# Kernel tuning notes

Hardware: AMD Instinct MI355X
Metric: run time of the kernel (lower is better)

## Reference

```python
import jax, jax.numpy as jnp
import numpy as np

H = 16   # heads
DK = 64  # d_model // heads
LN_EPS = 1e-5


def setup_inputs() -> dict:
    key = jax.random.key(0)
    ks = jax.random.split(key, 6)
    bs, S, D = 2, 1024, 1024
    lim = 1.0 / np.sqrt(DK)  # torch Linear default init scale
    return {
        "context": jax.random.normal(ks[0], (bs, S, D), jnp.float32),
        "eos_mask": jnp.ones((bs, 1, S, S), jnp.bool_),
        "prior": jax.random.uniform(ks[1], (bs, H, S, S), jnp.float32),
        "ln_w": jnp.ones((D,), jnp.float32),
        "ln_b": jnp.zeros((D,), jnp.float32),
        "wk": jax.random.uniform(ks[2], (DK, DK), jnp.float32, -lim, lim),
        "bk": jax.random.uniform(ks[3], (DK,), jnp.float32, -lim, lim),
        "wq": jax.random.uniform(ks[4], (DK, DK), jnp.float32, -lim, lim),
        "bq": jax.random.uniform(ks[5], (DK,), jnp.float32, -lim, lim),
    }


def reference(context, eos_mask, prior, ln_w, ln_b, wk, bk, wq, bq):
    bs, S, D = context.shape
    # LayerNorm (torch uses biased variance)
    mu = context.mean(-1, keepdims=True)
    var = context.var(-1, keepdims=True)
    x = (context - mu) / jnp.sqrt(var + LN_EPS) * ln_w + ln_b
    # [bs, h, S, dk]
    x = x.reshape(bs, S, H, DK).transpose(0, 2, 1, 3)

    a = jnp.eye(S, k=1, dtype=jnp.float32)    # superdiagonal
    c = jnp.eye(S, k=-1, dtype=jnp.float32)   # subdiagonal
    eye = jnp.eye(S, dtype=jnp.float32)
    mask = eos_mask & ((a + c) > 0)           # [bs,1,S,S] tridiagonal (no diag)

    k = x @ wk.T + bk
    q = x @ wq.T + bq
    scores = jnp.einsum('bhqd,bhkd->bhqk', q, k) / DK
    scores = jnp.where(mask, scores, -10000.0)
    neibor = jax.nn.softmax(scores, axis=-1)
    # symmetrized geometric-mean neighbor attention
    neibor = jnp.sqrt(neibor * jnp.swapaxes(neibor, -2, -1) + 1e-4)
    neibor = prior + (1.0 - prior) * neibor

    tri = jnp.triu(jnp.ones((S, S), jnp.float32))  # incl. diag
    # keep log only on the superdiagonal, then prefix-sum via triu matmuls
    logn = jnp.where(a > 0, jnp.log(neibor + 1e-9), 0.0)
    t = logn @ tri                      # [bs,h,S,S]
    g = jnp.exp(jnp.matmul(tri, t))     # broadcasted [S,S] @ [bs,h,S,S]
    g = jnp.where((tri - eye) > 0, g, 0.0)  # keep strict upper triangle
    g = g + jnp.swapaxes(g, -2, -1) + jnp.where(eye > 0, neibor, 1e-4)
    return g, neibor


if __name__ == "__main__":
    out = reference(**setup_inputs())
    print(out[0].shape, out[1].shape)
```

## Files before the change

### kernel.cpp

```cpp
#include <hip/hip_runtime.h>
#include <hip/hip_bf16.h>

#define S 1024
#define H 16
#define BS 2
#define D 1024

typedef float f32x4 __attribute__((ext_vector_type(4)));

__global__ __launch_bounds__(256) void k_ln_prep(const float* __restrict__ ctx,
                                                 const float* __restrict__ wk,
                                                 const float* __restrict__ bk,
                                                 const float* __restrict__ wq,
                                                 const float* __restrict__ bq,
                                                 float* __restrict__ mean,
                                                 float* __restrict__ rstd,
                                                 float* __restrict__ Mt,
                                                 float* __restrict__ uvec) {
    __shared__ float sh[2 * 64 * 65];
    int t = threadIdx.x;
    int bid = blockIdx.x;

    if (bid >= BS * S) {
        int p = bid - BS * S;
        float* WqL = sh;
        float* WkL = sh + 64 * 65;
        for (int idx = t; idx < 4096; idx += 256) {
            int d = idx >> 6, c = idx & 63;
            WqL[d * 65 + c] = wq[idx];
            WkL[d * 65 + c] = wk[idx];
        }
        __syncthreads();
        int a = t & 63, sub = t >> 6;
        for (int ee = sub; ee < 16; ee += 4) {
            int e = p * 16 + ee;
            float acc = 0.0f;
            #pragma unroll 8
            for (int d = 0; d < 64; ++d) acc += WqL[d * 65 + a] * WkL[d * 65 + e];
            Mt[e * 64 + a] = acc;
        }
        if (p == 0 && t < 64) {
            float acc = 0.0f;
            #pragma unroll 8
            for (int d = 0; d < 64; ++d) acc += bq[d] * WkL[d * 65 + t];
            uvec[t] = acc;
        }
        return;
    }

    const float* x = ctx + (size_t)bid * D;
    float4 v = *(const float4*)(x + t * 4);
    float s = v.x + v.y + v.z + v.w;
    float sq = v.x * v.x + v.y * v.y + v.z * v.z + v.w * v.w;
    #pragma unroll
    for (int off = 32; off > 0; off >>= 1) {
        s += __shfl_down(s, off);
        sq += __shfl_down(sq, off);
    }
    float* ss = sh;
    float* sqs = sh + 4;
    int w = t >> 6;
    if ((t & 63) == 0) { ss[w] = s; sqs[w] = sq; }
    __syncthreads();
    if (t == 0) {
        float sum = ss[0] + ss[1] + ss[2] + ss[3];
        float sumsq = sqs[0] + sqs[1] + sqs[2] + sqs[3];
        float m = sum * (1.0f / D);
        float var = sumsq * (1.0f / D) - m * m;
        mean[bid] = m;
        rstd[bid] = rsqrtf(var + 1e-5f);
    }
}

#define XST 68
__global__ __launch_bounds__(256) void k_scores(const float* __restrict__ ctx,
                                                const float* __restrict__ mean,
                                                const float* __restrict__ rstd,
                                                const float* __restrict__ lnw,
                                                const float* __restrict__ lnb,
                                                const float* __restrict__ Mt,
                                                const float* __restrict__ uvec,
                                                float* __restrict__ p_up,
                                                float* __restrict__ p_dn) {
    int chunk = blockIdx.x;
    int bh = blockIdx.y;
    int b = bh >> 4, h = bh & 15;
    int r0 = chunk * 64;
    int t = threadIdx.x;
    int lane = t & 63, w = t >> 6;

    __shared__ float xs[72][XST];
    __shared__ float ts[72][XST];

    float Mreg[64];
    #pragma unroll
    for (int e = 0; e < 64; ++e) Mreg[e] = Mt[e * 64 + lane];

    for (int idx = t; idx < 72 * 64; idx += 256) {
        int lr = idx >> 6, c = idx & 63;
        int row = r0 - 1 + lr;
        float v = 0.0f;
        if (lr < 66 && row >= 0 && row < S) {
            float cv = ctx[((size_t)b * S + row) * D + h * 64 + c];
            v = (cv - mean[b * S + row]) * rstd[b * S + row] * lnw[h * 64 + c] + lnb[h * 64 + c];
        }
        xs[lr][c] = v;
    }
    __syncthreads();

    for (int s8 = w; s8 < 9; s8 += 4) {
        int rb = s8 * 8;
        float acc[8] = {0, 0, 0, 0, 0, 0, 0, 0};
        #pragma unroll
        for (int eq = 0; eq < 16; ++eq) {
            #pragma unroll
            for (int rr = 0; rr < 8; ++rr) {
                float4 xv = *(const float4*)&xs[rb + rr][eq * 4];
                acc[rr] += Mreg[eq * 4 + 0] * xv.x + Mreg[eq * 4 + 1] * xv.y +
                           Mreg[eq * 4 + 2] * xv.z + Mreg[eq * 4 + 3] * xv.w;
            }
        }
        #pragma unroll
        for (int rr = 0; rr < 8; ++rr) ts[rb + rr][lane] = acc[rr];
    }
    __syncthreads();

    {
        int l = w * 16 + (lane >> 2);
        int part = lane & 3;
        float diff = 0.0f;
        #pragma unroll
        for (int dq = 0; dq < 4; ++dq) {
            int d0 = part * 16 + dq * 4;
            float4 xi = *(const float4*)&xs[l + 1][d0];
            float4 t2 = *(const float4*)&ts[l + 2][d0];
            float4 t0 = *(const float4*)&ts[l][d0];
            float4 x2 = *(const float4*)&xs[l + 2][d0];
            float4 x0 = *(const float4*)&xs[l][d0];
            float4 uv = *(const float4*)&uvec[d0];
            diff += xi.x * (t2.x - t0.x) + uv.x * (x2.x - x0.x);
            diff += xi.y * (t2.y - t0.y) + uv.y * (x2.y - x0.y);
            diff += xi.z * (t2.z - t0.z) + uv.z * (x2.z - x0.z);
            diff += xi.w * (t2.w - t0.w) + uv.w * (x2.w - x0.w);
        }
        diff += __shfl_down(diff, 2);
        diff += __shfl_down(diff, 1);
        if (part == 0) {
            int i = r0 + l;
            float z = diff * (1.0f / 64.0f);
            float pu, pd;
            if (i == 0)          { pu = 1.0f; pd = 0.0f; }
            else if (i == S - 1) { pu = 0.0f; pd = 1.0f; }
            else {
                float ez = __expf(-z);
                pu = 1.0f / (1.0f + ez);
                pd = 1.0f - pu;
            }
            p_up[bh * S + i] = pu;
            p_dn[bh * S + i] = pd;
        }
    }
}

__global__ __launch_bounds__(1024) void k_scan(const float* __restrict__ p_up,
                                               const float* __restrict__ p_dn,
                                               const float* __restrict__ prior,
                                               float* __restrict__ n_up,
                                               float* __restrict__ C) {
    int bh = blockIdx.x;
    int t = threadIdx.x;
    float L = 0.0f;
    if (t > 0) {
        int i = t - 1;
        float nr = sqrtf(p_up[bh * S + i] * p_dn[bh * S + i + 1] + 1e-4f);
        n_up[bh * S + i] = nr;
        float pr = prior[((size_t)bh * S + i) * S + i + 1];
        float N = pr + (1.0f - pr) * nr;
        L = logf(N + 1e-9f);
    }
    int lane = t & 63, wid = t >> 6;
    float val = L;
    #pragma unroll
    for (int off = 1; off < 64; off <<= 1) {
        float v = __shfl_up(val, off, 64);
        if (lane >= off) val += v;
    }
    __shared__ float wsum[16];
    if (lane == 63) wsum[wid] = val;
    __syncthreads();
    if (t < 16) {
        float v2 = wsum[t];
        #pragma unroll
        for (int off = 1; off < 16; off <<= 1) {
            float x = __shfl_up(v2, off, 64);
            if (t >= off) v2 += x;
        }
        wsum[t] = v2;
    }
    __syncthreads();
    float base = (wid > 0) ? wsum[wid - 1] : 0.0f;
    C[bh * S + t] = base + val;
}

__global__ __launch_bounds__(256) void k_out(const float* __restrict__ prior,
                                             const float* __restrict__ n_up,
                                             const float* __restrict__ C,
                                             float* __restrict__ g_out,
                                             float* __restrict__ nb_out) {
    int bid = blockIdx.x;
    int bh = bid >> 10, i = bid & 1023;
    int t = threadIdx.x;
    size_t rowbase = (size_t)bid * S;
    float Ci = C[bh * S + i];
    float nup_i  = (i < S - 1) ? n_up[bh * S + i] : 0.0f;
    float nup_im = (i > 0)     ? n_up[bh * S + i - 1] : 0.0f;
    int j0 = t * 4;
    f32x4 p4 = __builtin_nontemporal_load((const f32x4*)(prior + rowbase + j0));
    float4 c4 = *(const float4*)(C + bh * S + j0);
    float pv[4] = {p4.x, p4.y, p4.z, p4.w};
    float cv[4] = {c4.x, c4.y, c4.z, c4.w};
    float gv[4], nv[4];
    #pragma unroll
    for (int l = 0; l < 4; ++l) {
        int j = j0 + l;
        float p = pv[l];
        float v = 0.01f;
        if (j == i + 1) v = nup_i;
        if (j == i - 1) v = nup_im;
        float nb = p + (1.0f - p) * v;
        nv[l] = nb;
        float gg;
        if (j == i) {
            gg = nb;
        } else {
            float dd = (j > i) ? (cv[l] - Ci) : (Ci - cv[l]);
            gg = __expf(dd) + 1e-4f;
        }
        gv[l] = gg;
    }
    f32x4 gq = {gv[0], gv[1], gv[2], gv[3]};
    f32x4 nq = {nv[0], nv[1], nv[2], nv[3]};
    __builtin_nontemporal_store(gq, (f32x4*)(g_out + rowbase + j0));
    __builtin_nontemporal_store(nq, (f32x4*)(nb_out + rowbase + j0));
}

extern "C" void kernel_launch(void* const* d_in, const int* in_sizes, int n_in,
                              void* d_out, int out_size, void* d_ws, size_t ws_size,
                              hipStream_t stream) {
    const float* ctx   = (const float*)d_in[0];
    const float* prior = (const float*)d_in[2];
    const float* lnw   = (const float*)d_in[3];
    const float* lnb   = (const float*)d_in[4];
    const float* wk    = (const float*)d_in[5];
    const float* bk    = (const float*)d_in[6];
    const float* wq    = (const float*)d_in[7];
    const float* bq    = (const float*)d_in[8];

    float* ws = (float*)d_ws;
    float* mean = ws;
    float* rstd = ws + 2048;
    float* Mt   = ws + 4096;
    float* uvec = ws + 8192;
    float* p_up = ws + 8448;
    float* p_dn = ws + 8448 + 32768;
    float* n_up = ws + 8448 + 65536;
    float* C    = ws + 8448 + 98304;

    float* g_out  = (float*)d_out;
    float* nb_out = (float*)d_out + (size_t)BS * H * S * S;

    k_ln_prep<<<BS * S + 4, 256, 0, stream>>>(ctx, wk, bk, wq, bq, mean, rstd, Mt, uvec);
    k_scores<<<dim3(16, BS * H), 256, 0, stream>>>(ctx, mean, rstd, lnw, lnb, Mt, uvec,
                                                   p_up, p_dn);
    k_scan<<<BS * H, 1024, 0, stream>>>(p_up, p_dn, prior, n_up, C);
    k_out<<<BS * H * S, 256, 0, stream>>>(prior, n_up, C, g_out, nb_out);
}
```

Before: 106.0 us.

## Fuse LayerNorm, weight product and scores into one kernel; batch output rows

```diff
diff --git a/kernel.cpp b/kernel.cpp
--- a/kernel.cpp
+++ b/kernel.cpp
@@ -5,160 +5,142 @@
 #define H 16
 #define BS 2
 #define D 1024
+#define CH 8
 
 typedef float f32x4 __attribute__((ext_vector_type(4)));
 
-__global__ __launch_bounds__(256) void k_ln_prep(const float* __restrict__ ctx,
-                                                 const float* __restrict__ wk,
-                                                 const float* __restrict__ bk,
-                                                 const float* __restrict__ wq,
-                                                 const float* __restrict__ bq,
-                                                 float* __restrict__ mean,
-                                                 float* __restrict__ rstd,
-                                                 float* __restrict__ Mt,
-                                                 float* __restrict__ uvec) {
-    __shared__ float sh[2 * 64 * 65];
-    int t = threadIdx.x;
-    int bid = blockIdx.x;
-
-    if (bid >= BS * S) {
-        int p = bid - BS * S;
-        float* WqL = sh;
-        float* WkL = sh + 64 * 65;
-        for (int idx = t; idx < 4096; idx += 256) {
-            int d = idx >> 6, c = idx & 63;
-            WqL[d * 65 + c] = wq[idx];
-            WkL[d * 65 + c] = wk[idx];
-        }
-        __syncthreads();
-        int a = t & 63, sub = t >> 6;
-        for (int ee = sub; ee < 16; ee += 4) {
-            int e = p * 16 + ee;
-            float acc = 0.0f;
-            #pragma unroll 8
-            for (int d = 0; d < 64; ++d) acc += WqL[d * 65 + a] * WkL[d * 65 + e];
-            Mt[e * 64 + a] = acc;
-        }
-        if (p == 0 && t < 64) {
-            float acc = 0.0f;
-            #pragma unroll 8
-            for (int d = 0; d < 64; ++d) acc += bq[d] * WkL[d * 65 + t];
-            uvec[t] = acc;
-        }
-        return;
-    }
-
-    const float* x = ctx + (size_t)bid * D;
-    float4 v = *(const float4*)(x + t * 4);
-    float s = v.x + v.y + v.z + v.w;
-    float sq = v.x * v.x + v.y * v.y + v.z * v.z + v.w * v.w;
-    #pragma unroll
-    for (int off = 32; off > 0; off >>= 1) {
-        s += __shfl_down(s, off);
-        sq += __shfl_down(sq, off);
-    }
-    float* ss = sh;
-    float* sqs = sh + 4;
-    int w = t >> 6;
-    if ((t & 63) == 0) { ss[w] = s; sqs[w] = sq; }
-    __syncthreads();
-    if (t == 0) {
-        float sum = ss[0] + ss[1] + ss[2] + ss[3];
-        float sumsq = sqs[0] + sqs[1] + sqs[2] + sqs[3];
-        float m = sum * (1.0f / D);
-        float var = sumsq * (1.0f / D) - m * m;
-        mean[bid] = m;
-        rstd[bid] = rsqrtf(var + 1e-5f);
-    }
-}
-
-#define XST 68
-__global__ __launch_bounds__(256) void k_scores(const float* __restrict__ ctx,
-                                                const float* __restrict__ mean,
-                                                const float* __restrict__ rstd,
-                                                const float* __restrict__ lnw,
-                                                const float* __restrict__ lnb,
-                                                const float* __restrict__ Mt,
-                                                const float* __restrict__ uvec,
-                                                float* __restrict__ p_up,
-                                                float* __restrict__ p_dn) {
-    int chunk = blockIdx.x;
-    int bh = blockIdx.y;
-    int b = bh >> 4, h = bh & 15;
-    int r0 = chunk * 64;
+__global__ __launch_bounds__(256) void k12(const float* __restrict__ ctx,
+                                           const float* __restrict__ lnw,
+                                           const float* __restrict__ lnb,
+                                           const float* __restrict__ wk,
+                                           const float* __restrict__ wq,
+                                           const float* __restrict__ bq,
+                                           float* __restrict__ p_up,
+                                           float* __restrict__ p_dn) {
+    __shared__ float Ml[64 * 65];
+    __shared__ float uw[64];
+    __shared__ float xs[CH + 2][1032];
+    __shared__ float ts[CH + 2][68];
+    __shared__ float mu[CH + 2], rs[CH + 2];
+    __shared__ float lw[1024], lb[1024];
+
     int t = threadIdx.x;
     int lane = t & 63, w = t >> 6;
-
-    __shared__ float xs[72][XST];
-    __shared__ float ts[72][XST];
-
+    int chunk = blockIdx.x, b = blockIdx.y;
+    int r0 = chunk * CH;
+
+    float* WqL = &xs[0][0];
+    float* WkL = &xs[0][0] + 4160;
+    for (int idx = t; idx < 4096; idx += 256) {
+        int d = idx >> 6, c = idx & 63;
+        WqL[d * 65 + c] = wq[idx];
+        WkL[d * 65 + c] = wk[idx];
+    }
+    ((f32x4*)lw)[t] = ((const f32x4*)lnw)[t];
+    ((f32x4*)lb)[t] = ((const f32x4*)lnb)[t];
+    __syncthreads();
+    for (int ee = 0; ee < 16; ++ee) {
+        int e = w * 16 + ee;
+        float acc = 0.0f;
+        #pragma unroll 8
+        for (int d = 0; d < 64; ++d) acc += WqL[d * 65 + lane] * WkL[d * 65 + e];
+        Ml[e * 65 + lane] = acc;
+    }
+    if (w == 0) {
+        float acc = 0.0f;
+        #pragma unroll 8
+        for (int d = 0; d < 64; ++d) acc += bq[d] * WkL[d * 65 + lane];
+        uw[lane] = acc;
+    }
+    __syncthreads();
+
+    #pragma unroll
+    for (int q = 0; q < CH + 2; ++q) {
+        int gr = r0 - 1 + q;
+        f32x4 v = {0.f, 0.f, 0.f, 0.f};
+        if (gr >= 0 && gr < S) v = ((const f32x4*)(ctx + ((size_t)b * S + gr) * D))[t];
+        *(f32x4*)&xs[q][t * 4] = v;
+    }
     float Mreg[64];
     #pragma unroll
-    for (int e = 0; e < 64; ++e) Mreg[e] = Mt[e * 64 + lane];
-
-    for (int idx = t; idx < 72 * 64; idx += 256) {
-        int lr = idx >> 6, c = idx & 63;
-        int row = r0 - 1 + lr;
-        float v = 0.0f;
-        if (lr < 66 && row >= 0 && row < S) {
-            float cv = ctx[((size_t)b * S + row) * D + h * 64 + c];
-            v = (cv - mean[b * S + row]) * rstd[b * S + row] * lnw[h * 64 + c] + lnb[h * 64 + c];
-        }
-        xs[lr][c] = v;
-    }
-    __syncthreads();
-
-    for (int s8 = w; s8 < 9; s8 += 4) {
-        int rb = s8 * 8;
-        float acc[8] = {0, 0, 0, 0, 0, 0, 0, 0};
-        #pragma unroll
-        for (int eq = 0; eq < 16; ++eq) {
+    for (int e = 0; e < 64; ++e) Mreg[e] = Ml[e * 65 + lane];
+    __syncthreads();
+
+    for (int q = w; q < CH + 2; q += 4) {
+        float s = 0.f, sq = 0.f;
+        #pragma unroll
+        for (int k = 0; k < 4; ++k) {
+            f32x4 v = *(const f32x4*)&xs[q][(lane + 64 * k) * 4];
+            s += v.x + v.y + v.z + v.w;
+            sq += v.x * v.x + v.y * v.y + v.z * v.z + v.w * v.w;
+        }
+        #pragma unroll
+        for (int off = 32; off > 0; off >>= 1) {
+            s += __shfl_down(s, off);
+            sq += __shfl_down(sq, off);
+        }
+        if (lane == 0) {
+            float m = s * (1.0f / D);
+            float var = sq * (1.0f / D) - m * m;
+            mu[q] = m;
+            rs[q] = rsqrtf(var + 1e-5f);
+        }
+    }
+    __syncthreads();
+
+    #pragma unroll
+    for (int q = 0; q < CH + 2; ++q) {
+        float m = mu[q], r = rs[q];
+        f32x4 v = *(const f32x4*)&xs[q][t * 4];
+        f32x4 wv = *(const f32x4*)&lw[t * 4];
+        f32x4 bv = *(const f32x4*)&lb[t * 4];
+        v.x = (v.x - m) * r * wv.x + bv.x;
+        v.y = (v.y - m) * r * wv.y + bv.y;
+        v.z = (v.z - m) * r * wv.z + bv.z;
+        v.w = (v.w - m) * r * wv.w + bv.w;
+        *(f32x4*)&xs[q][t * 4] = v;
+    }
+    __syncthreads();
+
+    for (int h = 0; h < H; ++h) {
+        int hc = h * 64;
+        for (int q = w; q < CH + 2; q += 4) {
+            float a0 = 0.f, a1 = 0.f, a2 = 0.f, a3 = 0.f;
             #pragma unroll
-            for (int rr = 0; rr < 8; ++rr) {
-                float4 xv = *(const float4*)&xs[rb + rr][eq * 4];
-                acc[rr] += Mreg[eq * 4 + 0] * xv.x + Mreg[eq * 4 + 1] * xv.y +
-                           Mreg[eq * 4 + 2] * xv.z + Mreg[eq * 4 + 3] * xv.w;
+            for (int eq = 0; eq < 16; ++eq) {
+                f32x4 xv = *(const f32x4*)&xs[q][hc + eq * 4];
+                a0 += Mreg[eq * 4 + 0] * xv.x;
+                a1 += Mreg[eq * 4 + 1] * xv.y;
+                a2 += Mreg[eq * 4 + 2] * xv.z;
+                a3 += Mreg[eq * 4 + 3] * xv.w;
             }
-        }
-        #pragma unroll
-        for (int rr = 0; rr < 8; ++rr) ts[rb + rr][lane] = acc[rr];
-    }
-    __syncthreads();
-
-    {
-        int l = w * 16 + (lane >> 2);
-        int part = lane & 3;
-        float diff = 0.0f;
-        #pragma unroll
-        for (int dq = 0; dq < 4; ++dq) {
-            int d0 = part * 16 + dq * 4;
-            float4 xi = *(const float4*)&xs[l + 1][d0];
-            float4 t2 = *(const float4*)&ts[l + 2][d0];
-            float4 t0 = *(const float4*)&ts[l][d0];
-            float4 x2 = *(const float4*)&xs[l + 2][d0];
-            float4 x0 = *(const float4*)&xs[l][d0];
-            float4 uv = *(const float4*)&uvec[d0];
-            diff += xi.x * (t2.x - t0.x) + uv.x * (x2.x - x0.x);
-            diff += xi.y * (t2.y - t0.y) + uv.y * (x2.y - x0.y);
-            diff += xi.z * (t2.z - t0.z) + uv.z * (x2.z - x0.z);
-            diff += xi.w * (t2.w - t0.w) + uv.w * (x2.w - x0.w);
-        }
-        diff += __shfl_down(diff, 2);
-        diff += __shfl_down(diff, 1);
-        if (part == 0) {
-            int i = r0 + l;
-            float z = diff * (1.0f / 64.0f);
-            float pu, pd;
-            if (i == 0)          { pu = 1.0f; pd = 0.0f; }
-            else if (i == S - 1) { pu = 0.0f; pd = 1.0f; }
-            else {
-                float ez = __expf(-z);
-                pu = 1.0f / (1.0f + ez);
-                pd = 1.0f - pu;
+            ts[q][lane] = (a0 + a1) + (a2 + a3);
+        }
+        __syncthreads();
+        for (int lr = 1 + w; lr <= CH; lr += 4) {
+            int i = r0 + lr - 1;
+            float xi = xs[lr][hc + lane];
+            float tp = ts[lr + 1][lane] - ts[lr - 1][lane];
+            float xd = xs[lr + 1][hc + lane] - xs[lr - 1][hc + lane];
+            float v = xi * tp + uw[lane] * xd;
+            #pragma unroll
+            for (int off = 32; off > 0; off >>= 1) v += __shfl_down(v, off);
+            if (lane == 0) {
+                float z = v * (1.0f / 64.0f);
+                float pu, pd;
+                if (i == 0)          { pu = 1.0f; pd = 0.0f; }
+                else if (i == S - 1) { pu = 0.0f; pd = 1.0f; }
+                else {
+                    float ez = __expf(-z);
+                    pu = 1.0f / (1.0f + ez);
+                    pd = 1.0f - pu;
+                }
+                int bh = b * H + h;
+                p_up[bh * S + i] = pu;
+                p_dn[bh * S + i] = pd;
             }
-            p_up[bh * S + i] = pu;
-            p_dn[bh * S + i] = pd;
-        }
+        }
+        __syncthreads();
     }
 }
 
@@ -207,41 +189,41 @@
                                              const float* __restrict__ C,
                                              float* __restrict__ g_out,
                                              float* __restrict__ nb_out) {
+    int t = threadIdx.x;
     int bid = blockIdx.x;
-    int bh = bid >> 10, i = bid & 1023;
-    int t = threadIdx.x;
-    size_t rowbase = (size_t)bid * S;
-    float Ci = C[bh * S + i];
-    float nup_i  = (i < S - 1) ? n_up[bh * S + i] : 0.0f;
-    float nup_im = (i > 0)     ? n_up[bh * S + i - 1] : 0.0f;
+    int bh = bid >> 7;
+    int i0 = (bid & 127) * 8;
     int j0 = t * 4;
-    f32x4 p4 = __builtin_nontemporal_load((const f32x4*)(prior + rowbase + j0));
-    float4 c4 = *(const float4*)(C + bh * S + j0);
-    float pv[4] = {p4.x, p4.y, p4.z, p4.w};
-    float cv[4] = {c4.x, c4.y, c4.z, c4.w};
-    float gv[4], nv[4];
-    #pragma unroll
-    for (int l = 0; l < 4; ++l) {
-        int j = j0 + l;
-        float p = pv[l];
-        float v = 0.01f;
-        if (j == i + 1) v = nup_i;
-        if (j == i - 1) v = nup_im;
-        float nb = p + (1.0f - p) * v;
-        nv[l] = nb;
-        float gg;
-        if (j == i) {
-            gg = nb;
-        } else {
-            float dd = (j > i) ? (cv[l] - Ci) : (Ci - cv[l]);
-            gg = __expf(dd) + 1e-4f;
-        }
-        gv[l] = gg;
-    }
-    f32x4 gq = {gv[0], gv[1], gv[2], gv[3]};
-    f32x4 nq = {nv[0], nv[1], nv[2], nv[3]};
-    __builtin_nontemporal_store(gq, (f32x4*)(g_out + rowbase + j0));
-    __builtin_nontemporal_store(nq, (f32x4*)(nb_out + rowbase + j0));
+    const float* Crow = C + bh * S;
+    f32x4 c4 = *(const f32x4*)(Crow + j0);
+    f32x4 ciA = *(const f32x4*)(Crow + i0);
+    f32x4 ciB = *(const f32x4*)(Crow + i0 + 4);
+    #pragma unroll
+    for (int r = 0; r < 8; ++r) {
+        int i = i0 + r;
+        float Ci = (r < 4) ? ciA[r] : ciB[r - 4];
+        size_t rowbase = ((size_t)bh * S + i) * S;
+        f32x4 p4 = __builtin_nontemporal_load((const f32x4*)(prior + rowbase + j0));
+        f32x4 nb, gg;
+        #pragma unroll
+        for (int l = 0; l < 4; ++l) {
+            nb[l] = fmaf(0.99f, p4[l], 0.01f);
+            gg[l] = __expf(-fabsf(c4[l] - Ci)) + 1e-4f;
+        }
+        if (i - 1 <= j0 + 3 && i + 1 >= j0) {
+            float nup_i  = (i < S - 1) ? n_up[bh * S + i] : 0.0f;
+            float nup_im = (i > 0)     ? n_up[bh * S + i - 1] : 0.0f;
+            #pragma unroll
+            for (int l = 0; l < 4; ++l) {
+                int j = j0 + l;
+                if (j == i + 1) nb[l] = p4[l] + (1.0f - p4[l]) * nup_i;
+                if (j == i - 1) nb[l] = p4[l] + (1.0f - p4[l]) * nup_im;
+                if (j == i)     gg[l] = nb[l];
+            }
+        }
+        __builtin_nontemporal_store(gg, (f32x4*)(g_out + rowbase + j0));
+        __builtin_nontemporal_store(nb, (f32x4*)(nb_out + rowbase + j0));
+    }
 }
 
 extern "C" void kernel_launch(void* const* d_in, const int* in_sizes, int n_in,
@@ -252,26 +234,19 @@
     const float* lnw   = (const float*)d_in[3];
     const float* lnb   = (const float*)d_in[4];
     const float* wk    = (const float*)d_in[5];
-    const float* bk    = (const float*)d_in[6];
     const float* wq    = (const float*)d_in[7];
     const float* bq    = (const float*)d_in[8];
 
     float* ws = (float*)d_ws;
-    float* mean = ws;
-    float* rstd = ws + 2048;
-    float* Mt   = ws + 4096;
-    float* uvec = ws + 8192;
-    float* p_up = ws + 8448;
-    float* p_dn = ws + 8448 + 32768;
-    float* n_up = ws + 8448 + 65536;
-    float* C    = ws + 8448 + 98304;
+    float* p_up = ws;
+    float* p_dn = ws + 32768;
+    float* n_up = ws + 65536;
+    float* C    = ws + 98304;
 
     float* g_out  = (float*)d_out;
     float* nb_out = (float*)d_out + (size_t)BS * H * S * S;
 
-    k_ln_prep<<<BS * S + 4, 256, 0, stream>>>(ctx, wk, bk, wq, bq, mean, rstd, Mt, uvec);
-    k_scores<<<dim3(16, BS * H), 256, 0, stream>>>(ctx, mean, rstd, lnw, lnb, Mt, uvec,
-                                                   p_up, p_dn);
+    k12<<<dim3(S / CH, BS), 256, 0, stream>>>(ctx, lnw, lnb, wk, wq, bq, p_up, p_dn);
     k_scan<<<BS * H, 1024, 0, stream>>>(p_up, p_dn, prior, n_up, C);
-    k_out<<<BS * H * S, 256, 0, stream>>>(prior, n_up, C, g_out, nb_out);
-}
+    k_out<<<BS * H * S / 8, 256, 0, stream>>>(prior, n_up, C, g_out, nb_out);
+}
```

New measurement: 133.4 us. +25.8%, slower.

## Fuse neighbor log computation into scores kernel and batch 8 rows per output block

Applied to the files above, without the earlier changes.

```diff
diff --git a/kernel.cpp b/kernel.cpp
--- a/kernel.cpp
+++ b/kernel.cpp
@@ -10,7 +10,6 @@
 
 __global__ __launch_bounds__(256) void k_ln_prep(const float* __restrict__ ctx,
                                                  const float* __restrict__ wk,
-                                                 const float* __restrict__ bk,
                                                  const float* __restrict__ wq,
                                                  const float* __restrict__ bq,
                                                  float* __restrict__ mean,
@@ -80,8 +79,9 @@
                                                 const float* __restrict__ lnb,
                                                 const float* __restrict__ Mt,
                                                 const float* __restrict__ uvec,
-                                                float* __restrict__ p_up,
-                                                float* __restrict__ p_dn) {
+                                                const float* __restrict__ prior,
+                                                float* __restrict__ n_up,
+                                                float* __restrict__ Lg) {
     int chunk = blockIdx.x;
     int bh = blockIdx.y;
     int b = bh >> 4, h = bh & 15;
@@ -91,6 +91,7 @@
 
     __shared__ float xs[72][XST];
     __shared__ float ts[72][XST];
+    __shared__ float spu[66], spd[66];
 
     float Mreg[64];
     #pragma unroll
@@ -100,7 +101,7 @@
         int lr = idx >> 6, c = idx & 63;
         int row = r0 - 1 + lr;
         float v = 0.0f;
-        if (lr < 66 && row >= 0 && row < S) {
+        if (lr < 67 && row >= 0 && row < S) {
             float cv = ctx[((size_t)b * S + row) * D + h * 64 + c];
             v = (cv - mean[b * S + row]) * rstd[b * S + row] * lnw[h * 64 + c] + lnb[h * 64 + c];
         }
@@ -125,61 +126,67 @@
     }
     __syncthreads();
 
-    {
-        int l = w * 16 + (lane >> 2);
-        int part = lane & 3;
-        float diff = 0.0f;
-        #pragma unroll
-        for (int dq = 0; dq < 4; ++dq) {
-            int d0 = part * 16 + dq * 4;
-            float4 xi = *(const float4*)&xs[l + 1][d0];
-            float4 t2 = *(const float4*)&ts[l + 2][d0];
-            float4 t0 = *(const float4*)&ts[l][d0];
-            float4 x2 = *(const float4*)&xs[l + 2][d0];
-            float4 x0 = *(const float4*)&xs[l][d0];
-            float4 uv = *(const float4*)&uvec[d0];
-            diff += xi.x * (t2.x - t0.x) + uv.x * (x2.x - x0.x);
-            diff += xi.y * (t2.y - t0.y) + uv.y * (x2.y - x0.y);
-            diff += xi.z * (t2.z - t0.z) + uv.z * (x2.z - x0.z);
-            diff += xi.w * (t2.w - t0.w) + uv.w * (x2.w - x0.w);
-        }
-        diff += __shfl_down(diff, 2);
-        diff += __shfl_down(diff, 1);
-        if (part == 0) {
-            int i = r0 + l;
-            float z = diff * (1.0f / 64.0f);
-            float pu, pd;
-            if (i == 0)          { pu = 1.0f; pd = 0.0f; }
-            else if (i == S - 1) { pu = 0.0f; pd = 1.0f; }
-            else {
-                float ez = __expf(-z);
-                pu = 1.0f / (1.0f + ez);
-                pd = 1.0f - pu;
-            }
-            p_up[bh * S + i] = pu;
-            p_dn[bh * S + i] = pd;
-        }
-    }
-}
-
-__global__ __launch_bounds__(1024) void k_scan(const float* __restrict__ p_up,
-                                               const float* __restrict__ p_dn,
-                                               const float* __restrict__ prior,
-                                               float* __restrict__ n_up,
+    int part = lane & 3;
+    #pragma unroll
+    for (int pass = 0; pass < 2; ++pass) {
+        int l = pass == 0 ? (w * 16 + (lane >> 2)) : 64;
+        bool active = (pass == 0) || (w == 0 && (lane >> 2) == 0);
+        int i = r0 + l;
+        if (active && i < S) {
+            float diff = 0.0f;
+            #pragma unroll
+            for (int dq = 0; dq < 4; ++dq) {
+                int d0 = part * 16 + dq * 4;
+                float4 xi = *(const float4*)&xs[l + 1][d0];
+                float4 t2 = *(const float4*)&ts[l + 2][d0];
+                float4 t0 = *(const float4*)&ts[l][d0];
+                float4 x2 = *(const float4*)&xs[l + 2][d0];
+                float4 x0 = *(const float4*)&xs[l][d0];
+                float4 uv = *(const float4*)&uvec[d0];
+                diff += xi.x * (t2.x - t0.x) + uv.x * (x2.x - x0.x);
+                diff += xi.y * (t2.y - t0.y) + uv.y * (x2.y - x0.y);
+                diff += xi.z * (t2.z - t0.z) + uv.z * (x2.z - x0.z);
+                diff += xi.w * (t2.w - t0.w) + uv.w * (x2.w - x0.w);
+            }
+            diff += __shfl_down(diff, 2);
+            diff += __shfl_down(diff, 1);
+            if (part == 0) {
+                float z = diff * (1.0f / 64.0f);
+                float pu, pd;
+                if (i == 0)          { pu = 1.0f; pd = 0.0f; }
+                else if (i == S - 1) { pu = 0.0f; pd = 1.0f; }
+                else {
+                    float ez = __expf(-z);
+                    pu = 1.0f / (1.0f + ez);
+                    pd = 1.0f - pu;
+                }
+                spu[l] = pu;
+                spd[l] = pd;
+            }
+        }
+    }
+    __syncthreads();
+
+    if (t < 64) {
+        int i = r0 + t;
+        float L = 0.0f;
+        if (i < S - 1) {
+            float nr = sqrtf(spu[t] * spd[t + 1] + 1e-4f);
+            n_up[bh * S + i] = nr;
+            float pr = prior[((size_t)bh * S + i) * S + i + 1];
+            float N = pr + (1.0f - pr) * nr;
+            L = logf(N + 1e-9f);
+        }
+        Lg[bh * S + i] = L;
+    }
+}
+
+__global__ __launch_bounds__(1024) void k_scan(const float* __restrict__ Lg,
                                                float* __restrict__ C) {
     int bh = blockIdx.x;
     int t = threadIdx.x;
-    float L = 0.0f;
-    if (t > 0) {
-        int i = t - 1;
-        float nr = sqrtf(p_up[bh * S + i] * p_dn[bh * S + i + 1] + 1e-4f);
-        n_up[bh * S + i] = nr;
-        float pr = prior[((size_t)bh * S + i) * S + i + 1];
-        float N = pr + (1.0f - pr) * nr;
-        L = logf(N + 1e-9f);
-    }
+    float val = (t > 0) ? Lg[bh * S + t - 1] : 0.0f;
     int lane = t & 63, wid = t >> 6;
-    float val = L;
     #pragma unroll
     for (int off = 1; off < 64; off <<= 1) {
         float v = __shfl_up(val, off, 64);
@@ -207,41 +214,41 @@
                                              const float* __restrict__ C,
                                              float* __restrict__ g_out,
                                              float* __restrict__ nb_out) {
+    int t = threadIdx.x;
     int bid = blockIdx.x;
-    int bh = bid >> 10, i = bid & 1023;
-    int t = threadIdx.x;
-    size_t rowbase = (size_t)bid * S;
-    float Ci = C[bh * S + i];
-    float nup_i  = (i < S - 1) ? n_up[bh * S + i] : 0.0f;
-    float nup_im = (i > 0)     ? n_up[bh * S + i - 1] : 0.0f;
+    int bh = bid >> 7;
+    int i0 = (bid & 127) * 8;
     int j0 = t * 4;
-    f32x4 p4 = __builtin_nontemporal_load((const f32x4*)(prior + rowbase + j0));
-    float4 c4 = *(const float4*)(C + bh * S + j0);
-    float pv[4] = {p4.x, p4.y, p4.z, p4.w};
-    float cv[4] = {c4.x, c4.y, c4.z, c4.w};
-    float gv[4], nv[4];
-    #pragma unroll
-    for (int l = 0; l < 4; ++l) {
-        int j = j0 + l;
-        float p = pv[l];
-        float v = 0.01f;
-        if (j == i + 1) v = nup_i;
-        if (j == i - 1) v = nup_im;
-        float nb = p + (1.0f - p) * v;
-        nv[l] = nb;
-        float gg;
-        if (j == i) {
-            gg = nb;
-        } else {
-            float dd = (j > i) ? (cv[l] - Ci) : (Ci - cv[l]);
-            gg = __expf(dd) + 1e-4f;
-        }
-        gv[l] = gg;
-    }
-    f32x4 gq = {gv[0], gv[1], gv[2], gv[3]};
-    f32x4 nq = {nv[0], nv[1], nv[2], nv[3]};
-    __builtin_nontemporal_store(gq, (f32x4*)(g_out + rowbase + j0));
-    __builtin_nontemporal_store(nq, (f32x4*)(nb_out + rowbase + j0));
+    const float* Crow = C + bh * S;
+    f32x4 c4 = *(const f32x4*)(Crow + j0);
+    f32x4 ciA = *(const f32x4*)(Crow + i0);
+    f32x4 ciB = *(const f32x4*)(Crow + i0 + 4);
+    #pragma unroll
+    for (int r = 0; r < 8; ++r) {
+        int i = i0 + r;
+        float Ci = (r < 4) ? ciA[r] : ciB[r - 4];
+        size_t rowbase = ((size_t)bh * S + i) * S;
+        f32x4 p4 = __builtin_nontemporal_load((const f32x4*)(prior + rowbase + j0));
+        f32x4 nb, gg;
+        #pragma unroll
+        for (int l = 0; l < 4; ++l) {
+            nb[l] = fmaf(0.99f, p4[l], 0.01f);
+            gg[l] = __expf(-fabsf(c4[l] - Ci)) + 1e-4f;
+        }
+        if (i - 1 <= j0 + 3 && i + 1 >= j0) {
+            float nup_i  = (i < S - 1) ? n_up[bh * S + i] : 0.0f;
+            float nup_im = (i > 0)     ? n_up[bh * S + i - 1] : 0.0f;
+            #pragma unroll
+            for (int l = 0; l < 4; ++l) {
+                int j = j0 + l;
+                if (j == i + 1) nb[l] = p4[l] + (1.0f - p4[l]) * nup_i;
+                if (j == i - 1) nb[l] = p4[l] + (1.0f - p4[l]) * nup_im;
+                if (j == i)     gg[l] = nb[l];
+            }
+        }
+        __builtin_nontemporal_store(gg, (f32x4*)(g_out + rowbase + j0));
+        __builtin_nontemporal_store(nb, (f32x4*)(nb_out + rowbase + j0));
+    }
 }
 
 extern "C" void kernel_launch(void* const* d_in, const int* in_sizes, int n_in,
@@ -252,7 +259,6 @@
     const float* lnw   = (const float*)d_in[3];
     const float* lnb   = (const float*)d_in[4];
     const float* wk    = (const float*)d_in[5];
-    const float* bk    = (const float*)d_in[6];
     const float* wq    = (const float*)d_in[7];
     const float* bq    = (const float*)d_in[8];
 
@@ -261,17 +267,16 @@
     float* rstd = ws + 2048;
     float* Mt   = ws + 4096;
     float* uvec = ws + 8192;
-    float* p_up = ws + 8448;
-    float* p_dn = ws + 8448 + 32768;
-    float* n_up = ws + 8448 + 65536;
-    float* C    = ws + 8448 + 98304;
+    float* n_up = ws + 8448;
+    float* Lg   = ws + 8448 + 32768;
+    float* C    = ws + 8448 + 65536;
 
     float* g_out  = (float*)d_out;
     float* nb_out = (float*)d_out + (size_t)BS * H * S * S;
 
-    k_ln_prep<<<BS * S + 4, 256, 0, stream>>>(ctx, wk, bk, wq, bq, mean, rstd, Mt, uvec);
+    k_ln_prep<<<BS * S + 4, 256, 0, stream>>>(ctx, wk, wq, bq, mean, rstd, Mt, uvec);
     k_scores<<<dim3(16, BS * H), 256, 0, stream>>>(ctx, mean, rstd, lnw, lnb, Mt, uvec,
-                                                   p_up, p_dn);
-    k_scan<<<BS * H, 1024, 0, stream>>>(p_up, p_dn, prior, n_up, C);
-    k_out<<<BS * H * S, 256, 0, stream>>>(prior, n_up, C, g_out, nb_out);
-}
+                                                   prior, n_up, Lg);
+    k_scan<<<BS * H, 1024, 0, stream>>>(Lg, C);
+    k_out<<<BS * H * S / 8, 256, 0, stream>>>(prior, n_up, C, g_out, nb_out);
+}
```

Result: slower. 110.3 us (+4.0%).
